# Kernel optimization log

Measured on AMD Instinct MI355X. Metric: run time of the kernel, lower is better.

The kernel has to match this reference:

```python
import jax, jax.numpy as jnp
import numpy as np

SPARSITY = 0.5  # cur_sparsity set during training; 0.0 default would make masking a no-op
WEIGHT_BETA = 1.0
MASK_ALPHA1 = 1.0
MASK_ALPHA2 = 1.0


def binarize(mask_scores, sparsity):
    # SparseBinarizer.forward: prune (set to 0) the `num_prune` smallest scores globally.
    num_prune = int(mask_scores.size * sparsity)  # static: sparsity is a Python float
    flat = mask_scores.reshape(-1)
    prune_idx = jnp.argsort(flat)[:num_prune]
    mask = jnp.ones_like(flat).at[prune_idx].set(0.0)
    return mask.reshape(mask_scores.shape)


def setup_inputs() -> dict:
    key = jax.random.key(0)
    ks = jax.random.split(key, 9)
    out_f, in_f, r = 4096, 4096, 8
    tokens = 8192  # batch 4 * seq 2048
    return {
        "x": jax.random.normal(ks[0], (tokens, in_f), dtype=jnp.float32),
        "weight": jax.random.normal(ks[1], (out_f, in_f), dtype=jnp.float32) * 0.02,
        "bias": jax.random.normal(ks[2], (out_f,), dtype=jnp.float32) * 0.02,
        "weight_U": jax.random.normal(ks[3], (out_f, r), dtype=jnp.float32),
        "weight_V": jnp.zeros((r, in_f), dtype=jnp.float32),
        "mask_scores_A": jax.random.normal(ks[4], (out_f, r), dtype=jnp.float32),
        "mask_scores_B": jnp.zeros((r, in_f), dtype=jnp.float32),
        "mask_scores_R": jnp.zeros((out_f,), dtype=jnp.float32),
        "mask_scores_C": jnp.zeros((in_f,), dtype=jnp.float32),
    }


def reference(x, weight, bias, weight_U, weight_V, mask_scores_A, mask_scores_B,
              mask_scores_R, mask_scores_C):
    # weight = W + beta * U @ V   (low-rank weight reconstruction)
    w = weight + WEIGHT_BETA * (weight_U @ weight_V)
    # mask_scores = |w| + a1 * A @ B + a2 * (R[:,None] + C[None,:])
    mask_scores = (jnp.abs(w)
                   + MASK_ALPHA1 * (mask_scores_A @ mask_scores_B)
                   + MASK_ALPHA2 * (mask_scores_R[:, None] + mask_scores_C[None, :]))
    mask = binarize(mask_scores, SPARSITY)
    masked_weight = mask * w  # [out_f, in_f]
    # nn.Linear: x @ W^T + b
    return x @ masked_weight.T + bias
```

## Files before the change

### kernel.cpp

```cpp
#include <hip/hip_runtime.h>
#include <stdint.h>

#define TOKENS 8192
#define OUT_F  4096
#define IN_F   4096
#define RNK    8
#define RPB    4
#define KPRUNE 8388608u
#define CAP3   16384u

typedef unsigned short u16;
typedef float  f32x4  __attribute__((ext_vector_type(4)));
typedef short  bf16x8 __attribute__((ext_vector_type(8)));
typedef unsigned short u16x8 __attribute__((ext_vector_type(8)));

#define XB_OFF    0ull
#define WB_OFF    67108864ull
#define KEYS_OFF  100663296ull
#define CTL_OFF   167772160ull
#define H1_OFF    0
#define H2_OFF    16384
#define SEL_OFF   32768
#define CNT3_OFF  32800
#define LIST3_OFF 32804
#define CTL_ZERO_U32 8201

__device__ __forceinline__ u16 f2bf(float f) {
    uint32_t u = __float_as_uint(f);
    u += 0x7fffu + ((u >> 16) & 1u);
    return (u16)(u >> 16);
}

__device__ __forceinline__ uint32_t fkey(float s) {
    uint32_t u = __float_as_uint(s);
    return (u & 0x80000000u) ? ~u : (u | 0x80000000u);
}

__global__ void convx_kernel(const float* __restrict__ x, u16* __restrict__ xB,
                             uint32_t* __restrict__ ctl)
{
    const int t = threadIdx.x;
    if (blockIdx.x < 34) {
        const int i = blockIdx.x * 256 + t;
        if (i < CTL_ZERO_U32) ctl[i] = 0u;
    }
    const size_t idx = (size_t)blockIdx.x * 256 + t;
    const float4* xv = (const float4*)x;
    float4 a = xv[idx*2];
    float4 b = xv[idx*2 + 1];
    u16x8 o;
    o[0]=f2bf(a.x); o[1]=f2bf(a.y); o[2]=f2bf(a.z); o[3]=f2bf(a.w);
    o[4]=f2bf(b.x); o[5]=f2bf(b.y); o[6]=f2bf(b.z); o[7]=f2bf(b.w);
    *((u16x8*)xB + idx) = o;
}

__global__ void prep_kernel(const float* __restrict__ W, const float* __restrict__ U,
                            const float* __restrict__ V, const float* __restrict__ A,
                            const float* __restrict__ B, const float* __restrict__ R,
                            const float* __restrict__ C, u16* __restrict__ wB,
                            uint32_t* __restrict__ keys, uint32_t* __restrict__ hist1)
{
    __shared__ uint32_t lh[4096];
    const int o0 = blockIdx.x * RPB, t = threadIdx.x;
    for (int b = t; b < 4096; b += 256) lh[b] = 0u;
    float uu[RPB][RNK], aa[RPB][RNK], ro[RPB];
#pragma unroll
    for (int r0 = 0; r0 < RPB; ++r0) {
#pragma unroll
        for (int r = 0; r < RNK; ++r) {
            uu[r0][r] = U[(o0+r0)*RNK + r];
            aa[r0][r] = A[(o0+r0)*RNK + r];
        }
        ro[r0] = R[o0 + r0];
    }
    __syncthreads();
    for (int j = 0; j < IN_F/256; ++j) {
        const int i = j*256 + t;
        float vv[RNK], bb[RNK];
#pragma unroll
        for (int r = 0; r < RNK; ++r) { vv[r] = V[r*IN_F + i]; bb[r] = B[r*IN_F + i]; }
        const float ci = C[i];
#pragma unroll
        for (int r0 = 0; r0 < RPB; ++r0) {
            float wv = W[(size_t)(o0+r0)*IN_F + i];
#pragma unroll
            for (int r = 0; r < RNK; ++r) wv = fmaf(uu[r0][r], vv[r], wv);
            float s = fabsf(wv);
#pragma unroll
            for (int r = 0; r < RNK; ++r) s = fmaf(aa[r0][r], bb[r], s);
            s += ro[r0] + ci;
            const uint32_t key = fkey(s);
            keys[(size_t)(o0+r0)*IN_F + i] = key;
            wB[(size_t)(o0+r0)*IN_F + i]   = f2bf(wv);
            atomicAdd(&lh[key >> 20], 1u);
        }
    }
    __syncthreads();
    for (int b = t; b < 4096; b += 256) { uint32_t c = lh[b]; if (c) atomicAdd(&hist1[b], c); }
}

__global__ void select_kernel(const uint32_t* __restrict__ hist, uint32_t* sel, int mode)
{
    __shared__ uint32_t lh[4096];
    __shared__ uint32_t part[256];
    __shared__ uint32_t sseg[2];
    const int t = threadIdx.x;
    const uint32_t c1v = sel[1];
    const uint32_t k = (mode == 0) ? KPRUNE : (KPRUNE - c1v);
    for (int b = t; b < 4096; b += 256) lh[b] = hist[b];
    __syncthreads();
    uint32_t s = 0;
    for (int j = 0; j < 16; ++j) s += lh[t*16 + j];
    part[t] = s;
    __syncthreads();
    uint32_t pre = 0;
    for (int tt = 0; tt < t; ++tt) pre += part[tt];
    if (pre < k && pre + part[t] >= k) { sseg[0] = (uint32_t)t; sseg[1] = pre; }
    __syncthreads();
    const int seg = (int)sseg[0];
    const uint32_t accb = sseg[1];
    if (t < 16) {
        uint32_t pre2 = 0;
        for (int j = 0; j < t; ++j) pre2 += lh[seg*16 + j];
        const uint32_t c = lh[seg*16 + t];
        const uint32_t below = accb + pre2;
        if (below < k && below + c >= k) {
            const uint32_t bin = (uint32_t)(seg*16 + t);
            if (mode == 0) { sel[0] = bin; sel[1] = below; }
            else           { sel[2] = bin; sel[3] = c1v + below; }
        }
    }
}

__global__ void hist2_kernel(const uint32_t* __restrict__ keys, const uint32_t* __restrict__ sel,
                             uint32_t* __restrict__ hist2)
{
    __shared__ uint32_t lh[4096];
    const int o = blockIdx.x, t = threadIdx.x;
    const uint32_t b1 = sel[0];
    for (int b = t; b < 4096; b += 256) lh[b] = 0u;
    __syncthreads();
    const uint32_t* kp = keys + (size_t)o*IN_F + t*16;
#pragma unroll
    for (int q = 0; q < 4; ++q) {
        uint4 kv = *(const uint4*)(kp + q*4);
        if ((kv.x >> 20) == b1) atomicAdd(&lh[(kv.x >> 8) & 0xFFFu], 1u);
        if ((kv.y >> 20) == b1) atomicAdd(&lh[(kv.y >> 8) & 0xFFFu], 1u);
        if ((kv.z >> 20) == b1) atomicAdd(&lh[(kv.z >> 8) & 0xFFFu], 1u);
        if ((kv.w >> 20) == b1) atomicAdd(&lh[(kv.w >> 8) & 0xFFFu], 1u);
    }
    __syncthreads();
    for (int b = t; b < 4096; b += 256) { uint32_t c = lh[b]; if (c) atomicAdd(&hist2[b], c); }
}

__global__ void apply_kernel(const uint32_t* __restrict__ keys, const uint32_t* __restrict__ sel,
                             u16* __restrict__ wB, uint32_t* __restrict__ cnt3,
                             uint32_t* __restrict__ list3)
{
    const uint32_t pfx = (sel[0] << 12) | sel[2];
    const size_t base = ((size_t)blockIdx.x * 256 + threadIdx.x) * 16;
    uint32_t kv[16];
#pragma unroll
    for (int q = 0; q < 4; ++q) *(uint4*)(kv + q*4) = *(const uint4*)(keys + base + q*4);
    uint4 wraw[2];
    wraw[0] = *(const uint4*)(wB + base);
    wraw[1] = *(const uint4*)(wB + base + 8);
    u16* wv = (u16*)wraw;
#pragma unroll
    for (int e = 0; e < 16; ++e) {
        const uint32_t hi = kv[e] >> 8;
        if (hi < pfx) wv[e] = 0u;
        else if (hi == pfx) {
            uint32_t s = atomicAdd(cnt3, 1u);
            if (s < CAP3) list3[s] = ((uint32_t)(base + e) << 8) | (kv[e] & 0xFFu);
        }
    }
    *(uint4*)(wB + base)     = wraw[0];
    *(uint4*)(wB + base + 8) = wraw[1];
}

__global__ void selfix_kernel(const uint32_t* __restrict__ sel, const uint32_t* __restrict__ cnt3,
                              const uint32_t* __restrict__ list3, u16* __restrict__ wB)
{
    __shared__ uint32_t lst[CAP3];
    __shared__ uint32_t hist[256];
    __shared__ uint32_t sv[2];
    const int t = threadIdx.x;
    uint32_t n = *cnt3; if (n > CAP3) n = CAP3;
    hist[t] = 0u;
    __syncthreads();
    for (uint32_t i = t; i < n; i += 256) {
        const uint32_t e = list3[i];
        lst[i] = e;
        atomicAdd(&hist[e & 0xFFu], 1u);
    }
    __syncthreads();
    const uint32_t k3 = KPRUNE - sel[3];
    uint32_t pre = 0;
    for (int b = 0; b < t; ++b) pre += hist[b];
    if (pre < k3 && pre + hist[t] >= k3) {
        sv[0] = (uint32_t)t;
        sv[1] = k3 - pre;
    }
    __syncthreads();
    const uint32_t b3 = sv[0], p = sv[1];
    for (uint32_t i = t; i < n; i += 256) {
        const uint32_t e = lst[i];
        const uint32_t lo = e & 0xFFu;
        if (lo < b3) { wB[e >> 8] = 0u; continue; }
        if (lo != b3) continue;
        uint32_t rank = 0;
        for (uint32_t j = 0; j < n; ++j) {
            const uint32_t f = lst[j];
            rank += ((f & 0xFFu) == b3 && f < e) ? 1u : 0u;
        }
        if (rank < p) wB[e >> 8] = 0u;
    }
}

#define LA0 0
#define LB0 32768
#define LA1 65536
#define LB1 98304

__device__ __forceinline__ void gl_lds16(const char* src, char* dst) {
    __builtin_amdgcn_global_load_lds((const __attribute__((address_space(1))) void*)src,
                                     (__attribute__((address_space(3))) void*)dst, 16, 0, 0);
}

__global__ __launch_bounds__(512, 2) void gemm256_kernel(const u16* __restrict__ xB,
                                                         const u16* __restrict__ wB,
                                                         const float* __restrict__ bias,
                                                         float* __restrict__ out)
{
    __shared__ char ldsc[131072];
    const int t    = threadIdx.x;
    const int lane = t & 63;
    const int wid  = t >> 6;
    const int wm   = wid >> 2;
    const int wn   = wid & 3;
    const int bid  = blockIdx.x;
    const int bn   = bid & 15;
    const int bm   = bid >> 4;

    const int l15 = lane & 15;
    const int kb  = (lane >> 4) << 4;
    const int sw  = (lane & 7) << 4;
    const int bA  = (16*wm + l15) * 128 + kb;
    const int bB  = (64*wn + l15) * 128 + kb;

    const int scol = ((t & 7) * 16) ^ (((t >> 3) & 7) << 4);
    const char* pA = (const char*)xB + ((size_t)(bm*256 + (t >> 3))) * (IN_F*2) + scol;
    const char* pB = (const char*)wB + ((size_t)(bn*256 + (t >> 3))) * (IN_F*2) + scol;
    const int tb16 = t * 16;

#define STAGE(pG, reg, h, tile) do {                                          \
    const char* _s = (pG) + (size_t)(tile)*128 + (size_t)(h)*(128*IN_F*2);    \
    char* _d = ldsc + (reg) + (h)*16384 + tb16;                               \
    gl_lds16(_s, _d);                                                         \
    gl_lds16(_s + (size_t)(64*IN_F*2), _d + 8192);                            \
} while (0)

    f32x4  acc[8][4] = {};
    bf16x8 b[4][2];
    bf16x8 a[2][2];

#define LOADB(reg) do {                                                       \
    _Pragma("unroll") for (int ni = 0; ni < 4; ++ni)                          \
    _Pragma("unroll") for (int kk = 0; kk < 2; ++kk)                          \
        b[ni][kk] = *(const bf16x8*)(ldsc + (reg) +                           \
                      ((bB + ni*2048 + kk*64) ^ sw));                         \
} while (0)

#define LOADA(reg, q) do {                                                    \
    _Pragma("unroll") for (int mm = 0; mm < 2; ++mm)                          \
    _Pragma("unroll") for (int kk = 0; kk < 2; ++kk)                          \
        a[mm][kk] = *(const bf16x8*)(ldsc + (reg) +                           \
                      ((bA + (2*(q)+mm)*4096 + kk*64) ^ sw));                 \
} while (0)

#define MFMAQ(q) do {                                                         \
    _Pragma("unroll") for (int mm = 0; mm < 2; ++mm)                          \
    _Pragma("unroll") for (int ni = 0; ni < 4; ++ni)                          \
    _Pragma("unroll") for (int kk = 0; kk < 2; ++kk)                          \
        acc[2*(q)+mm][ni] = __builtin_amdgcn_mfma_f32_16x16x32_bf16(          \
            a[mm][kk], b[ni][kk], acc[2*(q)+mm][ni], 0, 0, 0);                \
} while (0)

#define PH_TAIL(q)                                                            \
    __builtin_amdgcn_s_barrier();                                             \
    asm volatile("s_waitcnt lgkmcnt(0)" ::: "memory");                        \
    __builtin_amdgcn_s_setprio(1);                                            \
    MFMAQ(q);                                                                 \
    __builtin_amdgcn_s_setprio(0);                                            \
    __builtin_amdgcn_s_barrier();

    STAGE(pB, LB0, 0, 0);
    STAGE(pB, LB0, 1, 0);
    STAGE(pA, LA0, 0, 0);
    STAGE(pA, LA0, 1, 0);
    STAGE(pB, LB1, 0, 1);
    STAGE(pB, LB1, 1, 1);
    STAGE(pA, LA1, 0, 1);
    asm volatile("s_waitcnt vmcnt(6)" ::: "memory");
    __builtin_amdgcn_s_barrier();

#pragma unroll 1
    for (int j = 0; j < IN_F/64/2; ++j) {
        const int to = 2*j + 1;
        const int se = (2*j + 2) & 63;
        const int so = (2*j + 3) & 63;

        LOADB(LB0); LOADA(LA0, 0);
        STAGE(pA, LA1, 1, to);
        asm volatile("s_waitcnt lgkmcnt(8)" ::: "memory");
        PH_TAIL(0)
        LOADA(LA0, 1);
        STAGE(pB, LB0, 0, se);
        PH_TAIL(1)
        LOADA(LA0, 2);
        STAGE(pB, LB0, 1, se);
        PH_TAIL(2)
        LOADA(LA0, 3);
        STAGE(pA, LA0, 0, se);
        asm volatile("s_waitcnt vmcnt(6)" ::: "memory");
        PH_TAIL(3)

        LOADB(LB1); LOADA(LA1, 0);
        STAGE(pA, LA0, 1, se);
        asm volatile("s_waitcnt lgkmcnt(8)" ::: "memory");
        PH_TAIL(0)
        LOADA(LA1, 1);
        STAGE(pB, LB1, 0, so);
        PH_TAIL(1)
        LOADA(LA1, 2);
        STAGE(pB, LB1, 1, so);
        PH_TAIL(2)
        LOADA(LA1, 3);
        STAGE(pA, LA1, 0, so);
        asm volatile("s_waitcnt vmcnt(6)" ::: "memory");
        PH_TAIL(3)
    }

    const int orow0 = bm*256 + 16*wm + ((lane >> 4) << 2);
    const int ocol0 = bn*256 + 64*wn + l15;
#pragma unroll
    for (int ni = 0; ni < 4; ++ni) {
        const int col = ocol0 + ni*16;
        const float bv = bias[col];
#pragma unroll
        for (int m = 0; m < 8; ++m) {
            const int r0 = orow0 + 32*m;
            f32x4 v = acc[m][ni];
#pragma unroll
            for (int q = 0; q < 4; ++q)
                __builtin_nontemporal_store(v[q] + bv, &out[(size_t)(r0 + q)*OUT_F + col]);
        }
    }
#undef STAGE
#undef LOADB
#undef LOADA
#undef MFMAQ
#undef PH_TAIL
}

extern "C" void kernel_launch(void* const* d_in, const int* in_sizes, int n_in,
                              void* d_out, int out_size, void* d_ws, size_t ws_size,
                              hipStream_t stream)
{
    const float* x    = (const float*)d_in[0];
    const float* W    = (const float*)d_in[1];
    const float* bias = (const float*)d_in[2];
    const float* U    = (const float*)d_in[3];
    const float* V    = (const float*)d_in[4];
    const float* A    = (const float*)d_in[5];
    const float* B    = (const float*)d_in[6];
    const float* R    = (const float*)d_in[7];
    const float* C    = (const float*)d_in[8];
    float* out = (float*)d_out;

    char* ws = (char*)d_ws;
    u16*      xB    = (u16*)(ws + XB_OFF);
    u16*      wB    = (u16*)(ws + WB_OFF);
    uint32_t* keys  = (uint32_t*)(ws + KEYS_OFF);
    uint32_t* ctl   = (uint32_t*)(ws + CTL_OFF);
    uint32_t* h1    = (uint32_t*)((char*)ctl + H1_OFF);
    uint32_t* h2    = (uint32_t*)((char*)ctl + H2_OFF);
    uint32_t* sel   = (uint32_t*)((char*)ctl + SEL_OFF);
    uint32_t* cnt3  = (uint32_t*)((char*)ctl + CNT3_OFF);
    uint32_t* list3 = (uint32_t*)((char*)ctl + LIST3_OFF);

    convx_kernel<<<TOKENS*IN_F/8/256, 256, 0, stream>>>(x, xB, ctl);
    prep_kernel<<<OUT_F/RPB, 256, 0, stream>>>(W, U, V, A, B, R, C, wB, keys, h1);
    select_kernel<<<1, 256, 0, stream>>>(h1, sel, 0);
    hist2_kernel<<<OUT_F, 256, 0, stream>>>(keys, sel, h2);
    select_kernel<<<1, 256, 0, stream>>>(h2, sel, 1);
    apply_kernel<<<OUT_F, 256, 0, stream>>>(keys, sel, wB, cnt3, list3);
    selfix_kernel<<<1, 256, 0, stream>>>(sel, cnt3, list3, wB);
    gemm256_kernel<<<(TOKENS/256)*(OUT_F/256), 512, 0, stream>>>(xB, wB, bias, out);
}
```

Before: 411.1 us.

## Double-buffer A upper half in LDS to prefetch one tile earlier

```diff
diff --git a/kernel.cpp b/kernel.cpp
--- a/kernel.cpp
+++ b/kernel.cpp
@@ -218,10 +218,14 @@
     }
 }
 
-#define LA0 0
-#define LB0 32768
-#define LA1 65536
-#define LB1 98304
+#define A0H0   0
+#define A0H1_0 16384
+#define A0H1_1 32768
+#define B0S    49152
+#define A1H0   81920
+#define A1H1_0 98304
+#define A1H1_1 114688
+#define B1S    131072
 
 __device__ __forceinline__ void gl_lds16(const char* src, char* dst) {
     __builtin_amdgcn_global_load_lds((const __attribute__((address_space(1))) void*)src,
@@ -233,7 +237,7 @@
                                                          const float* __restrict__ bias,
                                                          float* __restrict__ out)
 {
-    __shared__ char ldsc[131072];
+    __shared__ char ldsc[163840];
     const int t    = threadIdx.x;
     const int lane = t & 63;
     const int wid  = t >> 6;
@@ -246,7 +250,7 @@
     const int l15 = lane & 15;
     const int kb  = (lane >> 4) << 4;
     const int sw  = (lane & 7) << 4;
-    const int bA  = (16*wm + l15) * 128 + kb;
+    const int bAo = (16*wm + l15) * 128 + kb;
     const int bB  = (64*wn + l15) * 128 + kb;
 
     const int scol = ((t & 7) * 16) ^ (((t >> 3) & 7) << 4);
@@ -254,9 +258,9 @@
     const char* pB = (const char*)wB + ((size_t)(bn*256 + (t >> 3))) * (IN_F*2) + scol;
     const int tb16 = t * 16;
 
-#define STAGE(pG, reg, h, tile) do {                                          \
+#define STAGEH(pG, slot, h, tile) do {                                        \
     const char* _s = (pG) + (size_t)(tile)*128 + (size_t)(h)*(128*IN_F*2);    \
-    char* _d = ldsc + (reg) + (h)*16384 + tb16;                               \
+    char* _d = ldsc + (slot) + tb16;                                          \
     gl_lds16(_s, _d);                                                         \
     gl_lds16(_s + (size_t)(64*IN_F*2), _d + 8192);                            \
 } while (0)
@@ -272,11 +276,11 @@
                       ((bB + ni*2048 + kk*64) ^ sw));                         \
 } while (0)
 
-#define LOADA(reg, q) do {                                                    \
+#define LOADA(slot, q, mo) do {                                               \
     _Pragma("unroll") for (int mm = 0; mm < 2; ++mm)                          \
     _Pragma("unroll") for (int kk = 0; kk < 2; ++kk)                          \
-        a[mm][kk] = *(const bf16x8*)(ldsc + (reg) +                           \
-                      ((bA + (2*(q)+mm)*4096 + kk*64) ^ sw));                 \
+        a[mm][kk] = *(const bf16x8*)(ldsc + (slot) +                          \
+                      (((2*(q)+mm-(mo))*4096 + bAo + kk*64) ^ sw));           \
 } while (0)
 
 #define MFMAQ(q) do {                                                         \
@@ -295,50 +299,55 @@
     __builtin_amdgcn_s_setprio(0);                                            \
     __builtin_amdgcn_s_barrier();
 
-    STAGE(pB, LB0, 0, 0);
-    STAGE(pB, LB0, 1, 0);
-    STAGE(pA, LA0, 0, 0);
-    STAGE(pA, LA0, 1, 0);
-    STAGE(pB, LB1, 0, 1);
-    STAGE(pB, LB1, 1, 1);
-    STAGE(pA, LA1, 0, 1);
-    asm volatile("s_waitcnt vmcnt(6)" ::: "memory");
+    STAGEH(pA, A0H1_0, 1, 0);
+    STAGEH(pB, B0S,         0, 0);
+    STAGEH(pB, B0S + 16384, 1, 0);
+    STAGEH(pA, A0H0, 0, 0);
+    STAGEH(pA, A1H1_0, 1, 1);
+    STAGEH(pB, B1S,         0, 1);
+    STAGEH(pB, B1S + 16384, 1, 1);
+    STAGEH(pA, A1H0, 0, 1);
+    asm volatile("s_waitcnt vmcnt(8)" ::: "memory");
     __builtin_amdgcn_s_barrier();
 
 #pragma unroll 1
     for (int j = 0; j < IN_F/64/2; ++j) {
-        const int to = 2*j + 1;
         const int se = (2*j + 2) & 63;
         const int so = (2*j + 3) & 63;
-
-        LOADB(LB0); LOADA(LA0, 0);
-        STAGE(pA, LA1, 1, to);
+        const int pc = j & 1;
+        const int a0h1c = pc ? A0H1_1 : A0H1_0;
+        const int a0h1n = pc ? A0H1_0 : A0H1_1;
+        const int a1h1c = pc ? A1H1_1 : A1H1_0;
+        const int a1h1n = pc ? A1H1_0 : A1H1_1;
+
+        LOADB(B0S); LOADA(A0H0, 0, 0);
+        STAGEH(pA, a0h1n, 1, se);
         asm volatile("s_waitcnt lgkmcnt(8)" ::: "memory");
         PH_TAIL(0)
-        LOADA(LA0, 1);
-        STAGE(pB, LB0, 0, se);
+        LOADA(A0H0, 1, 0);
+        STAGEH(pB, B0S, 0, se);
         PH_TAIL(1)
-        LOADA(LA0, 2);
-        STAGE(pB, LB0, 1, se);
+        LOADA(a0h1c, 2, 4);
+        STAGEH(pB, B0S + 16384, 1, se);
         PH_TAIL(2)
-        LOADA(LA0, 3);
-        STAGE(pA, LA0, 0, se);
-        asm volatile("s_waitcnt vmcnt(6)" ::: "memory");
+        LOADA(a0h1c, 3, 4);
+        STAGEH(pA, A0H0, 0, se);
+        asm volatile("s_waitcnt vmcnt(8)" ::: "memory");
         PH_TAIL(3)
 
-        LOADB(LB1); LOADA(LA1, 0);
-        STAGE(pA, LA0, 1, se);
+        LOADB(B1S); LOADA(A1H0, 0, 0);
+        STAGEH(pA, a1h1n, 1, so);
         asm volatile("s_waitcnt lgkmcnt(8)" ::: "memory");
         PH_TAIL(0)
-        LOADA(LA1, 1);
-        STAGE(pB, LB1, 0, so);
+        LOADA(A1H0, 1, 0);
+        STAGEH(pB, B1S, 0, so);
         PH_TAIL(1)
-        LOADA(LA1, 2);
-        STAGE(pB, LB1, 1, so);
+        LOADA(a1h1c, 2, 4);
+        STAGEH(pB, B1S + 16384, 1, so);
         PH_TAIL(2)
-        LOADA(LA1, 3);
-        STAGE(pA, LA1, 0, so);
-        asm volatile("s_waitcnt vmcnt(6)" ::: "memory");
+        LOADA(a1h1c, 3, 4);
+        STAGEH(pA, A1H0, 0, so);
+        asm volatile("s_waitcnt vmcnt(8)" ::: "memory");
         PH_TAIL(3)
     }
 
@@ -354,10 +363,10 @@
             f32x4 v = acc[m][ni];
 #pragma unroll
             for (int q = 0; q < 4; ++q)
-                __builtin_nontemporal_store(v[q] + bv, &out[(size_t)(r0 + q)*OUT_F + col]);
-        }
-    }
-#undef STAGE
+                out[(size_t)(r0 + q)*OUT_F + col] = v[q] + bv;
+        }
+    }
+#undef STAGEH
 #undef LOADB
 #undef LOADA
 #undef MFMAQ
```

Result: slower. 423.8 us (+3.1%).
